# Kernel tuning notes

Hardware: AMD Instinct MI355X
Metric: run time of the kernel (lower is better)

Reference implementation:

```python
import math
import jax, jax.numpy as jnp
import numpy as np


def setup_inputs() -> dict:
    key = jax.random.key(0)
    ks = jax.random.split(key, 6)
    b, k, t, h = 4, 128, 2048, 8
    s = 0.05
    return {
        "x": jax.random.normal(ks[0], (b, k, t), dtype=jnp.float32),
        "Wq": jax.random.normal(ks[1], (h * k, k), dtype=jnp.float32) * s,
        "Wk": jax.random.normal(ks[2], (h * k, k), dtype=jnp.float32) * s,
        "Wv": jax.random.normal(ks[3], (h * k, k), dtype=jnp.float32) * s,
        "Wu": jax.random.normal(ks[4], (k, h * k), dtype=jnp.float32) * s,
        "bu": jax.random.normal(ks[5], (k,), dtype=jnp.float32) * s,
    }


def reference(x, Wq, Wk, Wv, Wu, bu):
    b, k, t = x.shape
    h = Wq.shape[0] // k

    def proj(W):
        # x: [b,k,t], W: [h*k, k] -> [b,h,k,t]
        return jnp.einsum('bkt,jk->bjt', x, W).reshape(b, h, k, t)

    q = proj(Wq)
    keys = proj(Wk)
    v = proj(Wv)

    # scores: [b,h,t,t], scaled by 1/sqrt(k)
    dot = jnp.einsum('bhkt,bhki->bhti', q, keys) / math.sqrt(k)
    attn = jax.nn.softmax(dot, axis=-1)

    # attend: [b,h,k,t]
    o = jnp.einsum('bhti,bhki->bhkt', attn, v)

    # unify heads: Wu [k, h*k] viewed as [k,h,k]
    Wu3 = Wu.reshape(k, h, k)
    out = jnp.einsum('bhet,khe->bkt', o, Wu3)
    return out + bu[None, :, None]
```

## Files before the change

### kernel.cpp

```cpp
#include <hip/hip_runtime.h>
#include <hip/hip_bf16.h>

using short8 = __attribute__((ext_vector_type(8))) short;
using f32x4  = __attribute__((ext_vector_type(4))) float;
using f32x16 = __attribute__((ext_vector_type(16))) float;
using uint2v = __attribute__((ext_vector_type(2))) unsigned;

#define B_  4
#define KD  128
#define T_  2048
#define H_  8
#define HK  (H_*KD)
#define NT  (T_/64)
#define VROW 72

__device__ __forceinline__ ushort f2bf(float f) {
    unsigned u = __builtin_bit_cast(unsigned, f);
    u += 0x7fffu + ((u >> 16) & 1u);
    return (ushort)(u >> 16);
}

__device__ __forceinline__ float exp2_hw(float x) {
    float r;
    asm("v_exp_f32 %0, %1" : "=v"(r) : "v"(x));
    return r;
}

__device__ __forceinline__ unsigned cvt_pk_fp8_lo(unsigned old, float a, float b) {
    unsigned r = old;
    asm("v_cvt_pk_fp8_f32 %0, %1, %2" : "+v"(r) : "v"(a), "v"(b));
    return r;
}
__device__ __forceinline__ unsigned cvt_pk_fp8_hi(unsigned old, float a, float b) {
    unsigned r = old;
    asm("v_cvt_pk_fp8_f32 %0, %1, %2 op_sel:[0,0,1]" : "+v"(r) : "v"(a), "v"(b));
    return r;
}

__global__ __launch_bounds__(256) void prep_kernel(const float* __restrict__ x,
                                                   const float* __restrict__ Wq,
                                                   const float* __restrict__ Wk,
                                                   const float* __restrict__ Wv,
                                                   const float* __restrict__ Wu,
                                                   ushort* __restrict__ wdst,
                                                   ushort* __restrict__ xt) {
    __shared__ float tile[64][65];
    int bx = blockIdx.x;
    if (bx < 2048) {
        int i = bx * 256 + threadIdx.x;
        const int n1 = HK * KD;
        const float* src = (i < n1) ? Wq : (i < 2*n1) ? Wk : (i < 3*n1) ? Wv : Wu;
        wdst[i] = f2bf(src[i & (n1 - 1)]);
        return;
    }
    int bi = bx - 2048;
    int t0 = (bi & 31) * 64;
    int k0 = ((bi >> 5) & 1) * 64;
    int b  = bi >> 6;
    int c  = threadIdx.x & 63;
    int r4 = threadIdx.x >> 6;
    #pragma unroll
    for (int i = 0; i < 16; i++) {
        int k = r4 * 16 + i;
        tile[k][c] = x[((size_t)b * KD + k0 + k) * T_ + t0 + c];
    }
    __syncthreads();
    #pragma unroll
    for (int i = 0; i < 16; i++) {
        int t = r4 * 16 + i;
        xt[((size_t)b * T_ + t0 + t) * KD + k0 + c] = f2bf(tile[c][t]);
    }
}

__global__ __launch_bounds__(256, 2) void proj_kernel(const ushort* __restrict__ xt,
                                                      const ushort* __restrict__ wall,
                                                      ushort* __restrict__ qtb,
                                                      ushort* __restrict__ ktb,
                                                      unsigned char* __restrict__ vsb) {
    int bz = blockIdx.y;
    int which = bz >> 2, b = bz & 3;
    int tidb = blockIdx.x;
    int lane = threadIdx.x & 63;
    int w    = threadIdx.x >> 6;
    int lq = lane & 31, hi = lane >> 5, hi8 = hi * 8;

    int tt0 = (tidb >> 3) * 128;
    int jj0 = (tidb & 7) * 128;

    const ushort *a0p, *a1p, *b0p, *b1p;
    int m0, n0;
    if (which < 2) {
        m0 = jj0 + (w >> 1) * 64;
        n0 = tt0 + (w & 1) * 64;
        const ushort* A  = wall + (size_t)which * (HK * KD);
        const ushort* Bp = xt + (size_t)b * T_ * KD;
        a0p = A  + (size_t)(m0 + lq) * KD + hi8;
        a1p = A  + (size_t)(m0 + 32 + lq) * KD + hi8;
        b0p = Bp + (size_t)(n0 + lq) * KD + hi8;
        b1p = Bp + (size_t)(n0 + 32 + lq) * KD + hi8;
    } else {
        m0 = tt0 + (w >> 1) * 64;
        n0 = jj0 + (w & 1) * 64;
        const ushort* A  = xt + (size_t)b * T_ * KD;
        const ushort* Bp = wall + (size_t)2 * (HK * KD);
        a0p = A  + (size_t)(m0 + lq) * KD + hi8;
        a1p = A  + (size_t)(m0 + 32 + lq) * KD + hi8;
        b0p = Bp + (size_t)(n0 + lq) * KD + hi8;
        b1p = Bp + (size_t)(n0 + 32 + lq) * KD + hi8;
    }

    short8 a0[8], a1[8], b0[8], b1[8];
    #pragma unroll
    for (int kc = 0; kc < 8; kc++) {
        a0[kc] = *(const short8*)(a0p + kc * 16);
        a1[kc] = *(const short8*)(a1p + kc * 16);
        b0[kc] = *(const short8*)(b0p + kc * 16);
        b1[kc] = *(const short8*)(b1p + kc * 16);
    }
    f32x16 acc[2][2] = {};
    #pragma unroll
    for (int kc = 0; kc < 8; kc++) {
        acc[0][0] = __builtin_amdgcn_mfma_f32_32x32x16_bf16(a0[kc], b0[kc], acc[0][0], 0, 0, 0);
        acc[0][1] = __builtin_amdgcn_mfma_f32_32x32x16_bf16(a0[kc], b1[kc], acc[0][1], 0, 0, 0);
        acc[1][0] = __builtin_amdgcn_mfma_f32_32x32x16_bf16(a1[kc], b0[kc], acc[1][0], 0, 0, 0);
        acc[1][1] = __builtin_amdgcn_mfma_f32_32x32x16_bf16(a1[kc], b1[kc], acc[1][1], 0, 0, 0);
    }

    if (which < 2) {
        float scale = which ? 1.f : 0.12751743f;
        ushort* C = (which ? ktb : qtb) + (size_t)b * T_ * HK;
        #pragma unroll
        for (int i = 0; i < 2; i++)
            #pragma unroll
            for (int jj = 0; jj < 2; jj++) {
                int t = n0 + jj*32 + lq;
                #pragma unroll
                for (int qd = 0; qd < 4; qd++) {
                    int jb = m0 + i*32 + 8*qd + 4*hi;
                    const f32x16& a = acc[i][jj];
                    unsigned u0 = (unsigned)f2bf(a[4*qd+0]*scale)
                                | ((unsigned)f2bf(a[4*qd+1]*scale) << 16);
                    unsigned u1 = (unsigned)f2bf(a[4*qd+2]*scale)
                                | ((unsigned)f2bf(a[4*qd+3]*scale) << 16);
                    uint2v uv; uv[0] = u0; uv[1] = u1;
                    *(uint2v*)(C + (size_t)t * HK + jb) = uv;
                }
            }
    } else {
        unsigned char* C = vsb + (size_t)b * HK * T_;
        #pragma unroll
        for (int i = 0; i < 2; i++)
            #pragma unroll
            for (int jj = 0; jj < 2; jj++) {
                int j = n0 + jj*32 + lq;
                #pragma unroll
                for (int qd = 0; qd < 4; qd++) {
                    int tb = m0 + i*32 + 8*qd + 4*hi;
                    const f32x16& a = acc[i][jj];
                    unsigned dw = cvt_pk_fp8_lo(0u, a[4*qd+0], a[4*qd+1]);
                    dw = cvt_pk_fp8_hi(dw, a[4*qd+2], a[4*qd+3]);
                    *(unsigned*)(C + (size_t)j * T_ + tb) = dw;
                }
            }
    }
}

__global__ __launch_bounds__(256) void gemm_abT_f32bias(const ushort* __restrict__ A,
                                                        const ushort* __restrict__ B, long sB,
                                                        const float* __restrict__ bias,
                                                        float* __restrict__ C, long sC,
                                                        int M, int N, int Kd) {
    int b = blockIdx.z;
    B += (long)b * sB;  C += (long)b * sC;
    int lane = threadIdx.x & 63;
    int w    = threadIdx.x >> 6;
    int lr = lane & 15, lg = lane >> 4;
    int m0 = blockIdx.x * 64 + (w >> 1) * 32;
    int n0 = blockIdx.y * 64 + (w & 1) * 32;

    f32x4 acc[2][2] = {};
    #pragma unroll 4
    for (int k0 = 0; k0 < Kd; k0 += 32) {
        short8 af[2], bf[2];
        #pragma unroll
        for (int i = 0; i < 2; i++)
            af[i] = *(const short8*)(A + (long)(m0 + i*16 + lr) * Kd + k0 + lg*8);
        #pragma unroll
        for (int j = 0; j < 2; j++)
            bf[j] = *(const short8*)(B + (long)(n0 + j*16 + lr) * Kd + k0 + lg*8);
        #pragma unroll
        for (int i = 0; i < 2; i++)
            #pragma unroll
            for (int j = 0; j < 2; j++)
                acc[i][j] = __builtin_amdgcn_mfma_f32_16x16x32_bf16(af[i], bf[j], acc[i][j], 0, 0, 0);
    }
    #pragma unroll
    for (int i = 0; i < 2; i++)
        #pragma unroll
        for (int j = 0; j < 2; j++)
            #pragma unroll
            for (int r = 0; r < 4; r++) {
                int m = m0 + i*16 + lg*4 + r;
                int n = n0 + j*16 + lr;
                C[(long)m * N + n] = acc[i][j][r] + bias[m];
            }
}

__global__ __launch_bounds__(512, 2) void attn32_kernel(const ushort* __restrict__ qt,
                                                        const ushort* __restrict__ kt,
                                                        const unsigned char* __restrict__ vs,
                                                        ushort* __restrict__ ot) {
    int f = blockIdx.x;
    int xcd = f & 7, u = f >> 3;
    int qt8 = u & 7, gh = u >> 3;
    int g = xcd + 8 * gh;
    int h = g & 7, b = g >> 3;
    int w    = threadIdx.x >> 6;
    int lane = threadIdx.x & 63;
    int lq = lane & 31, hi = lane >> 5;
    int hi8 = hi * 8;
    int q0w = qt8 * 256 + w * 32;

    __shared__ __align__(16) ushort k_lds[2][64 * 128];
    __shared__ __align__(16) unsigned char v_lds[2][128 * VROW];

    int tid  = threadIdx.x;
    int krow = tid >> 3, kcol = (tid & 7) << 4;
    const ushort* kst = kt + ((size_t)b * T_ + krow) * HK + h * KD + kcol;
    int kwi = krow * 128 + (kcol ^ ((krow & 7) << 3));
    int vrow = tid >> 2, vc16 = (tid & 3) << 4;
    const unsigned char* vst = vs + ((size_t)b * HK + h * KD + vrow) * T_ + vc16;
    int vwb = vrow * VROW + ((((vc16 >> 4) ^ (vrow & 3))) << 4);

    const ushort* qbase = qt + ((size_t)b * T_ + q0w + lq) * HK + h * KD + hi8;

    short8 qf[8];
    #pragma unroll
    for (int dc = 0; dc < 8; dc++)
        qf[dc] = *(const short8*)(qbase + dc * 16);

    short8 rk0 = *(const short8*)(kst);
    short8 rk1 = *(const short8*)(kst + 8);
    long rvlo = *(const long*)(vst);
    long rvhi = *(const long*)(vst + 8);
    *(short8*)&k_lds[0][kwi]     = rk0;
    *(short8*)&k_lds[0][kwi ^ 8] = rk1;
    *(long*)&v_lds[0][vwb]       = rvlo;
    *(long*)&v_lds[0][vwb + 8]   = rvhi;
    rk0 = *(const short8*)(kst + (size_t)64 * HK);
    rk1 = *(const short8*)(kst + (size_t)64 * HK + 8);
    rvlo = *(const long*)(vst + 64);
    rvhi = *(const long*)(vst + 64 + 8);
    __syncthreads();

    f32x16 o_acc[4] = {};
    float m_q = -1e30f, l_q = 0.f;
    const int xsw = (lq & 7) << 3;
    const int vsw = lq & 3;

    for (int t = 0; t < NT; ++t) {
        const int cur = t & 1;
        f32x16 s0 = {}, s1 = {};
        const ushort* kr0 = &k_lds[cur][(size_t)lq * 128];
        const ushort* kr1 = &k_lds[cur][(size_t)(32 + lq) * 128];
        #pragma unroll
        for (int dc = 0; dc < 8; dc++) {
            int c = (dc * 16 + hi8) ^ xsw;
            short8 kf0 = *(const short8*)(kr0 + c);
            short8 kf1 = *(const short8*)(kr1 + c);
            s0 = __builtin_amdgcn_mfma_f32_32x32x16_bf16(kf0, qf[dc], s0, 0, 0, 0);
            s1 = __builtin_amdgcn_mfma_f32_32x32x16_bf16(kf1, qf[dc], s1, 0, 0, 0);
        }

        float mx[8];
        #pragma unroll
        for (int i = 0; i < 8; i++)
            mx[i] = fmaxf(fmaxf(s0[i], s0[i+8]), fmaxf(s1[i], s1[i+8]));
        #pragma unroll
        for (int st = 4; st > 0; st >>= 1)
            #pragma unroll
            for (int i = 0; i < st; i++) mx[i] = fmaxf(mx[i], mx[i+st]);
        float pmax = fmaxf(mx[0], __shfl_xor(mx[0], 32));

        if (!__all(pmax - m_q <= 7.f)) {
            float mnew = fmaxf(m_q, pmax);
            float corr = exp2_hw(m_q - mnew);
            l_q *= corr;
            m_q = mnew;
            #pragma unroll
            for (int r = 0; r < 16; r++) {
                float cr = __shfl(corr, (r & 3) + 8 * (r >> 2) + 4 * hi);
                #pragma unroll
                for (int dn = 0; dn < 4; dn++) o_acc[dn][r] *= cr;
            }
        }

        float ls0 = 0.f, ls1 = 0.f, ls2 = 0.f, ls3 = 0.f;
        #pragma unroll
        for (int r = 0; r < 16; r++) {
            float e0 = exp2_hw(s0[r] - m_q);
            float e1 = exp2_hw(s1[r] - m_q);
            s0[r] = e0; s1[r] = e1;
            if (r & 1) { ls1 += e0; ls3 += e1; } else { ls0 += e0; ls2 += e1; }
        }
        float lsum = (ls0 + ls1) + (ls2 + ls3);
        lsum += __shfl_xor(lsum, 32);
        l_q += lsum;

        long ap8[4];
        #pragma unroll
        for (int ks = 0; ks < 4; ks++) {
            const f32x16& sN = (ks < 2) ? s0 : s1;
            int rb = (ks & 1) * 8;
            unsigned F0 = cvt_pk_fp8_lo(0u, sN[rb+0], sN[rb+1]);
            F0 = cvt_pk_fp8_hi(F0, sN[rb+2], sN[rb+3]);
            unsigned F1 = cvt_pk_fp8_lo(0u, sN[rb+4], sN[rb+5]);
            F1 = cvt_pk_fp8_hi(F1, sN[rb+6], sN[rb+7]);
            uint2v d01 = __builtin_amdgcn_permlane32_swap(F0, F1, false, false);
            ap8[ks] = (long)(((unsigned long)d01[1] << 32) | (unsigned long)d01[0]);
        }

        #pragma unroll
        for (int dn = 0; dn < 4; dn++) {
            const unsigned char* vr = &v_lds[cur][(size_t)(dn*32 + lq) * VROW];
            #pragma unroll
            for (int ks = 0; ks < 4; ks++) {
                long vf = *(const long*)(vr + ((ks ^ vsw) << 4) + hi8);
                o_acc[dn] = __builtin_amdgcn_mfma_f32_32x32x16_fp8_fp8(ap8[ks], vf, o_acc[dn], 0, 0, 0);
            }
        }

        __syncthreads();
        if (t + 1 < NT) {
            const int nxt = cur ^ 1;
            *(short8*)&k_lds[nxt][kwi]     = rk0;
            *(short8*)&k_lds[nxt][kwi ^ 8] = rk1;
            *(long*)&v_lds[nxt][vwb]       = rvlo;
            *(long*)&v_lds[nxt][vwb + 8]   = rvhi;
            if (t + 2 < NT) {
                size_t ko = (size_t)(t + 2) * 64 * HK;
                int    vo = (t + 2) * 64;
                rk0 = *(const short8*)(kst + ko);
                rk1 = *(const short8*)(kst + ko + 8);
                rvlo = *(const long*)(vst + vo);
                rvhi = *(const long*)(vst + vo + 8);
            }
            __syncthreads();
        }
    }

    float linv = 1.f / l_q;
    ushort* ob = ot + ((size_t)b * T_ + q0w) * HK + h * KD;
    #pragma unroll
    for (int r = 0; r < 16; r++) {
        int qrow = (r & 3) + 8 * (r >> 2) + 4 * hi;
        float lr_ = __shfl(linv, qrow);
        #pragma unroll
        for (int dn = 0; dn < 4; dn++)
            ob[(size_t)qrow * HK + dn*32 + lq] = f2bf(o_acc[dn][r] * lr_);
    }
}

extern "C" void kernel_launch(void* const* d_in, const int* in_sizes, int n_in,
                              void* d_out, int out_size, void* d_ws, size_t ws_size,
                              hipStream_t stream) {
    const float* x  = (const float*)d_in[0];
    const float* Wq = (const float*)d_in[1];
    const float* Wk = (const float*)d_in[2];
    const float* Wv = (const float*)d_in[3];
    const float* Wu = (const float*)d_in[4];
    const float* bu = (const float*)d_in[5];
    float* out = (float*)d_out;

    const size_t XT  = (size_t)B_ * T_ * KD * 2;
    const size_t WB  = (size_t)HK * KD * 2;
    const size_t BIG = (size_t)B_ * T_ * HK * 2;
    const size_t VSZ = (size_t)B_ * HK * T_;
    size_t need = XT + 4*WB + 3*BIG + VSZ;
    if (ws_size < need) return;

    char* p = (char*)d_ws;
    ushort* xt  = (ushort*)p;            p += XT;
    ushort* wqb = (ushort*)p;            p += WB;
    ushort* wkb = (ushort*)p;            p += WB;
    ushort* wvb = (ushort*)p;            p += WB;
    ushort* wub = (ushort*)p;            p += WB;
    ushort* qtb = (ushort*)p;            p += BIG;
    ushort* ktb = (ushort*)p;            p += BIG;
    unsigned char* vsb = (unsigned char*)p;  p += VSZ;
    ushort* otb = (ushort*)p;            p += BIG;
    (void)wkb; (void)wvb;

    prep_kernel<<<2304, 256, 0, stream>>>(x, Wq, Wk, Wv, Wu, wqb, xt);

    proj_kernel<<<dim3(128, 12), 256, 0, stream>>>(xt, wqb, qtb, ktb, vsb);

    attn32_kernel<<<dim3(256), 512, 0, stream>>>(qtb, ktb, vsb, otb);

    gemm_abT_f32bias<<<dim3(KD/64, T_/64, B_), 256, 0, stream>>>(
        wub, otb, (long)T_*HK, bu, out, (long)KD*T_, KD, T_, HK);
}
```

Baseline: 125.6 us.

## Load K tiles via global_load_lds and drop the second barrier per iteration

The attention kernel now streams K tiles straight from global memory into LDS with global_load_lds, keeping the XOR swizzle by pre-swizzling source addresses. The K load is issued at the top of each iteration and the V register-to-LDS store is moved to right after the QK MFMAs, which removes the second __syncthreads per tile and frees the K staging registers. The projection kernel also remaps its block index to change tile traversal order for locality. The risk is that async LDS writes have no explicit vmcnt wait before the single barrier, so correctness depends on the compiler inserting one.

Result: slower. 129.6 us (+3.2%).

```diff
diff --git a/kernel.cpp b/kernel.cpp
--- a/kernel.cpp
+++ b/kernel.cpp
@@ -13,6 +13,9 @@
 #define HK  (H_*KD)
 #define NT  (T_/64)
 #define VROW 72
+
+typedef const __attribute__((address_space(1))) char glob_char;
+typedef __attribute__((address_space(3))) char lds_char;
 
 __device__ __forceinline__ ushort f2bf(float f) {
     unsigned u = __builtin_bit_cast(unsigned, f);
@@ -79,7 +82,8 @@
                                                       unsigned char* __restrict__ vsb) {
     int bz = blockIdx.y;
     int which = bz >> 2, b = bz & 3;
-    int tidb = blockIdx.x;
+    int bxr = blockIdx.x;
+    int tidb = (bxr & 7) * 16 + (bxr >> 3);
     int lane = threadIdx.x & 63;
     int w    = threadIdx.x >> 6;
     int lq = lane & 31, hi = lane >> 5, hi8 = hi * 8;
@@ -225,9 +229,13 @@
     __shared__ __align__(16) unsigned char v_lds[2][128 * VROW];
 
     int tid  = threadIdx.x;
-    int krow = tid >> 3, kcol = (tid & 7) << 4;
-    const ushort* kst = kt + ((size_t)b * T_ + krow) * HK + h * KD + kcol;
-    int kwi = krow * 128 + (kcol ^ ((krow & 7) << 3));
+    const char* kgb = (const char*)(kt + ((size_t)b * T_) * HK + h * KD);
+    int krow_base = w * 8 + (lane >> 4);
+    int kp = lane & 15;
+    size_t ksrc0 = (size_t)krow_base * (HK * 2) + (size_t)((kp ^ (krow_base & 7)) << 4);
+    int krow1 = krow_base + 4;
+    size_t ksrc1 = (size_t)krow1 * (HK * 2) + (size_t)((kp ^ (krow1 & 7)) << 4);
+
     int vrow = tid >> 2, vc16 = (tid & 3) << 4;
     const unsigned char* vst = vs + ((size_t)b * HK + h * KD + vrow) * T_ + vc16;
     int vwb = vrow * VROW + ((((vc16 >> 4) ^ (vrow & 3))) << 4);
@@ -239,16 +247,18 @@
     for (int dc = 0; dc < 8; dc++)
         qf[dc] = *(const short8*)(qbase + dc * 16);
 
-    short8 rk0 = *(const short8*)(kst);
-    short8 rk1 = *(const short8*)(kst + 8);
+    {
+        glob_char* g0 = (glob_char*)(kgb + ksrc0);
+        glob_char* g1 = (glob_char*)(kgb + ksrc1);
+        lds_char* d0 = (lds_char*)((char*)&k_lds[0][0] + (w*2 + 0) * 1024);
+        lds_char* d1 = (lds_char*)((char*)&k_lds[0][0] + (w*2 + 1) * 1024);
+        __builtin_amdgcn_global_load_lds(g0, d0, 16, 0, 0);
+        __builtin_amdgcn_global_load_lds(g1, d1, 16, 0, 0);
+    }
     long rvlo = *(const long*)(vst);
     long rvhi = *(const long*)(vst + 8);
-    *(short8*)&k_lds[0][kwi]     = rk0;
-    *(short8*)&k_lds[0][kwi ^ 8] = rk1;
     *(long*)&v_lds[0][vwb]       = rvlo;
     *(long*)&v_lds[0][vwb + 8]   = rvhi;
-    rk0 = *(const short8*)(kst + (size_t)64 * HK);
-    rk1 = *(const short8*)(kst + (size_t)64 * HK + 8);
     rvlo = *(const long*)(vst + 64);
     rvhi = *(const long*)(vst + 64 + 8);
     __syncthreads();
@@ -260,6 +270,17 @@
 
     for (int t = 0; t < NT; ++t) {
         const int cur = t & 1;
+        const int nxt = cur ^ 1;
+        if (t + 1 < NT) {
+            size_t tb = (size_t)(t + 1) * 64 * (HK * 2);
+            glob_char* g0 = (glob_char*)(kgb + tb + ksrc0);
+            glob_char* g1 = (glob_char*)(kgb + tb + ksrc1);
+            lds_char* d0 = (lds_char*)((char*)&k_lds[nxt][0] + (w*2 + 0) * 1024);
+            lds_char* d1 = (lds_char*)((char*)&k_lds[nxt][0] + (w*2 + 1) * 1024);
+            __builtin_amdgcn_global_load_lds(g0, d0, 16, 0, 0);
+            __builtin_amdgcn_global_load_lds(g1, d1, 16, 0, 0);
+        }
+
         f32x16 s0 = {}, s1 = {};
         const ushort* kr0 = &k_lds[cur][(size_t)lq * 128];
         const ushort* kr1 = &k_lds[cur][(size_t)(32 + lq) * 128];
@@ -270,6 +291,16 @@
             short8 kf1 = *(const short8*)(kr1 + c);
             s0 = __builtin_amdgcn_mfma_f32_32x32x16_bf16(kf0, qf[dc], s0, 0, 0, 0);
             s1 = __builtin_amdgcn_mfma_f32_32x32x16_bf16(kf1, qf[dc], s1, 0, 0, 0);
+        }
+
+        if (t + 1 < NT) {
+            *(long*)&v_lds[nxt][vwb]     = rvlo;
+            *(long*)&v_lds[nxt][vwb + 8] = rvhi;
+            if (t + 2 < NT) {
+                int vo = (t + 2) * 64;
+                rvlo = *(const long*)(vst + vo);
+                rvhi = *(const long*)(vst + vo + 8);
+            }
         }
 
         float mx[8];
@@ -331,22 +362,6 @@
         }
 
         __syncthreads();
-        if (t + 1 < NT) {
-            const int nxt = cur ^ 1;
-            *(short8*)&k_lds[nxt][kwi]     = rk0;
-            *(short8*)&k_lds[nxt][kwi ^ 8] = rk1;
-            *(long*)&v_lds[nxt][vwb]       = rvlo;
-            *(long*)&v_lds[nxt][vwb + 8]   = rvhi;
-            if (t + 2 < NT) {
-                size_t ko = (size_t)(t + 2) * 64 * HK;
-                int    vo = (t + 2) * 64;
-                rk0 = *(const short8*)(kst + ko);
-                rk1 = *(const short8*)(kst + ko + 8);
-                rvlo = *(const long*)(vst + vo);
-                rvhi = *(const long*)(vst + vo + 8);
-            }
-            __syncthreads();
-        }
     }
 
     float linv = 1.f / l_q;
```
